# Performance work log

Hardware: AMD Instinct MI355X
Metric: run time of the kernel (lower is better)

Reference implementation:

```python
import jax, jax.numpy as jnp
import numpy as np

MAX_WORDS = 256  # = batch['labels'].shape[1]


def _align(hidden, word_ids, max_words):
    """Batched segment-mean: (B,S,D) subtoken states -> (B,max_words,D) word states.
    Equivalent to align_subtokens_to_words applied per sample (word_ids all valid)."""
    B, S, D = hidden.shape
    seg = (word_ids.astype(jnp.int32) + jnp.arange(B, dtype=jnp.int32)[:, None] * max_words).reshape(-1)
    sums = jax.ops.segment_sum(hidden.reshape(-1, D), seg, num_segments=B * max_words)
    cnts = jax.ops.segment_sum(jnp.ones((B * S,), hidden.dtype), seg, num_segments=B * max_words)
    out = jnp.where(cnts[:, None] > 0, sums / jnp.maximum(cnts, 1.0)[:, None], 0.0)
    return out.reshape(B, max_words, D)


def setup_inputs() -> dict:
    key = jax.random.key(0)
    ks = jax.random.split(key, 8)
    B, S, D, W = 64, 512, 768, MAX_WORDS
    h_hing_sub = jax.random.normal(ks[0], (B, S, D), dtype=jnp.float32)
    h_rob_sub = jax.random.normal(ks[1], (B, S, D), dtype=jnp.float32)
    hing_word_ids = jnp.sort(jax.random.randint(ks[2], (B, S), 0, W), axis=-1).astype(jnp.int32)
    rob_word_ids = jnp.sort(jax.random.randint(ks[3], (B, S), 0, W), axis=-1).astype(jnp.int32)
    num_words = jax.random.randint(ks[4], (B,), 1, W).astype(jnp.int32)
    router_w1 = jax.random.normal(ks[5], (2 * D, 256), dtype=jnp.float32) * (1.0 / np.sqrt(2 * D))
    router_b1 = jnp.zeros((256,), jnp.float32)
    router_w2 = jax.random.normal(ks[6], (256, 1), dtype=jnp.float32) * (1.0 / 16.0)
    router_b2 = jnp.zeros((1,), jnp.float32)
    head_w = jax.random.normal(ks[7], (D, 7), dtype=jnp.float32) * (1.0 / np.sqrt(D))
    head_b = jnp.zeros((7,), jnp.float32)
    return {
        'h_hing_sub': h_hing_sub, 'h_rob_sub': h_rob_sub,
        'hing_word_ids': hing_word_ids, 'rob_word_ids': rob_word_ids,
        'num_words': num_words,
        'router_w1': router_w1, 'router_b1': router_b1,
        'router_w2': router_w2, 'router_b2': router_b2,
        'head_w': head_w, 'head_b': head_b,
    }


def reference(h_hing_sub, h_rob_sub, hing_word_ids, rob_word_ids, num_words,
              router_w1, router_b1, router_w2, router_b2, head_w, head_b):
    W = MAX_WORDS
    # scatter-mean subtokens -> words (the dominant custom-kernel op)
    h_hing = _align(h_hing_sub, hing_word_ids, W)   # (B, W, 768)
    h_rob = _align(h_rob_sub, rob_word_ids, W)      # (B, W, 768)
    # token-level MLP router on concatenated word states (router_input='both')
    router_in = jnp.concatenate([h_hing, h_rob], axis=-1)             # (B, W, 1536)
    hdn = jax.nn.relu(jnp.einsum('bwd,dh->bwh', router_in, router_w1) + router_b1)
    alpha = jax.nn.sigmoid(jnp.einsum('bwh,ho->bwo', hdn, router_w2) + router_b2)  # (B, W, 1)
    blended = alpha * h_hing + (1.0 - alpha) * h_rob                  # (B, W, 768)
    logits = jnp.einsum('bwd,dl->bwl', blended, head_w) + head_b      # (B, W, num_labels)
    l2_disagreement = jnp.linalg.norm(h_hing - h_rob, axis=-1)        # (B, W)
    return logits, alpha.squeeze(-1), l2_disagreement
```

## Files before the change

kernel.cpp:

```cpp
#include <hip/hip_runtime.h>
#include <hip/hip_bf16.h>
#include <math.h>

#define BATCH 64
#define SEQ   512
#define DIM   768
#define NW    256
#define NT    (BATCH * NW)
#define KDIM  1536
#define HID   256
#define NL    7

#define BM  32
#define BK  64
#define BKP 72
#define NKT (KDIM / BK)

typedef __bf16 bf16_t;
typedef bf16_t bf16x4 __attribute__((ext_vector_type(4)));
typedef bf16_t bf16x8 __attribute__((ext_vector_type(8)));
typedef float  f32x4  __attribute__((ext_vector_type(4)));

__global__ __launch_bounds__(256) void prep_kernel(
    const float* __restrict__ w1, bf16_t* __restrict__ w1t,
    const int* __restrict__ idh, const int* __restrict__ idr,
    int* __restrict__ starts)
{
    if (blockIdx.x < 192) {
        int kc = blockIdx.x >> 3;
        int kg = blockIdx.x & 7;
        int n  = threadIdx.x;
        bf16x8 v;
        #pragma unroll
        for (int j = 0; j < 8; j++)
            v[j] = (bf16_t)w1[(size_t)(kc * 64 + kg * 8 + j) * HID + n];
        *(bf16x8*)(w1t + (size_t)kc * (HID * BK) + n * BK + kg * 8) = v;
    } else {
        int blk = blockIdx.x - 192;
        int t = blk >> 6;
        int b = blk & 63;
        const int* ids = (t ? idr : idh) + b * SEQ;
        int w = threadIdx.x;
        int lo = 0, hi = SEQ;
        while (lo < hi) {
            int m = (lo + hi) >> 1;
            if (ids[m] < w) lo = m + 1; else hi = m;
        }
        int* row = starts + blk * 257;
        row[w] = lo;
        if (w == 0) row[256] = SEQ;
    }
}

__global__ __launch_bounds__(256) void align_kernel(
    const float* __restrict__ hh, const float* __restrict__ hr,
    const int* __restrict__ starts, bf16_t* __restrict__ X)
{
    int tid  = threadIdx.x;
    int lane = tid & 63;
    int wv   = tid >> 6;
    int task = blockIdx.x * 4 + wv;
    int w    = task & 255;
    int t    = (task >> 8) & 1;
    int b    = task >> 9;

    const int* st = starts + (t * 64 + b) * 257;
    int lo = __builtin_amdgcn_readfirstlane(st[w]);
    int hi = __builtin_amdgcn_readfirstlane(st[w + 1]);
    int n  = hi - lo;

    const f32x4* src = (const f32x4*)((t ? hr : hh) + (size_t)b * SEQ * DIM) + lane;
    bf16_t*      xr  = X + (size_t)b * NW * KDIM + (size_t)w * KDIM + t * DIM;

    f32x4 a0 = {0.f,0.f,0.f,0.f}, a1 = a0, a2 = a0;
    for (int s = lo; s < hi; s++) {
        const f32x4* r = src + (size_t)s * 192;
        f32x4 v0 = r[0];
        f32x4 v1 = r[64];
        f32x4 v2 = r[128];
        a0 += v0; a1 += v1; a2 += v2;
    }
    float inv = n > 0 ? 1.0f / (float)n : 0.0f;
    bf16x4 o0, o1, o2;
    #pragma unroll
    for (int e = 0; e < 4; e++) {
        o0[e] = (bf16_t)(a0[e] * inv);
        o1[e] = (bf16_t)(a1[e] * inv);
        o2[e] = (bf16_t)(a2[e] * inv);
    }
    *(bf16x4*)(xr + lane * 4)         = o0;
    *(bf16x4*)(xr + (lane + 64) * 4)  = o1;
    *(bf16x4*)(xr + (lane + 128) * 4) = o2;
}

__global__ __launch_bounds__(256) void gemm_blend_kernel(
    const bf16_t* __restrict__ X, const bf16_t* __restrict__ w1t,
    const float* __restrict__ b1, const float* __restrict__ w2,
    const float* __restrict__ b2, const float* __restrict__ hw,
    const float* __restrict__ hb, float* __restrict__ out)
{
    __shared__ __align__(16) unsigned char smem[4608 + 36864];
    bf16_t (*Xs)[BKP] = (bf16_t (*)[BKP])smem;
    bf16_t (*Ws)[BKP] = (bf16_t (*)[BKP])(smem + 4608);
    float*  hws       = (float*)(smem + 4608);
    __shared__ float alpha_acc[BM];
    __shared__ float alpha_s[BM];

    int tid   = threadIdx.x;
    int lane  = tid & 63;
    int wv    = tid >> 6;
    int row16 = lane & 15;
    int quad  = lane >> 4;
    int tok0  = blockIdx.x * BM;

    f32x4 acc[2][4];
    #pragma unroll
    for (int mi = 0; mi < 2; mi++)
        #pragma unroll
        for (int ni = 0; ni < 4; ni++)
            acc[mi][ni] = (f32x4){0.f, 0.f, 0.f, 0.f};

    int xr = tid >> 3;
    int xc = tid & 7;

    for (int kc = 0; kc < NKT; kc++) {
        {
            const uint4* src = (const uint4*)(X + (size_t)(tok0 + xr) * KDIM + kc * BK + xc * 8);
            *(uint4*)(&Xs[xr][xc * 8]) = *src;
        }
        {
            const uint4* srcb = (const uint4*)(w1t + (size_t)kc * (HID * BK));
            #pragma unroll
            for (int i = 0; i < 8; i++) {
                int cidx = tid + i * 256;
                *(uint4*)(&Ws[cidx >> 3][(cidx & 7) * 8]) = srcb[cidx];
            }
        }
        __syncthreads();
        #pragma unroll
        for (int kk2 = 0; kk2 < 2; kk2++) {
            bf16x8 af[2], bfg[4];
            #pragma unroll
            for (int mi = 0; mi < 2; mi++)
                af[mi] = *(const bf16x8*)(&Xs[mi * 16 + row16][kk2 * 32 + quad * 8]);
            #pragma unroll
            for (int ni = 0; ni < 4; ni++)
                bfg[ni] = *(const bf16x8*)(&Ws[wv * 64 + ni * 16 + row16][kk2 * 32 + quad * 8]);
            #pragma unroll
            for (int mi = 0; mi < 2; mi++)
                #pragma unroll
                for (int ni = 0; ni < 4; ni++)
                    acc[mi][ni] = __builtin_amdgcn_mfma_f32_16x16x32_bf16(
                        af[mi], bfg[ni], acc[mi][ni], 0, 0, 0);
        }
        __syncthreads();
    }

    float w2v[4], b1v[4];
    #pragma unroll
    for (int ni = 0; ni < 4; ni++) {
        int col = wv * 64 + ni * 16 + row16;
        w2v[ni] = w2[col];
        b1v[ni] = b1[col];
    }
    if (tid < BM) alpha_acc[tid] = 0.f;
    __syncthreads();

    #pragma unroll
    for (int mi = 0; mi < 2; mi++) {
        #pragma unroll
        for (int r = 0; r < 4; r++) {
            float p = 0.f;
            #pragma unroll
            for (int ni = 0; ni < 4; ni++) {
                float v = acc[mi][ni][r] + b1v[ni];
                v = v > 0.f ? v : 0.f;
                p += v * w2v[ni];
            }
            p += __shfl_xor(p, 1);
            p += __shfl_xor(p, 2);
            p += __shfl_xor(p, 4);
            p += __shfl_xor(p, 8);
            if (row16 == 0)
                atomicAdd(&alpha_acc[mi * 16 + quad * 4 + r], p);
        }
    }

    for (int i = tid; i < DIM * NL; i += 256) {
        int d = i / NL, l = i - d * NL;
        hws[l * DIM + d] = hw[i];
    }
    __syncthreads();

    if (tid < BM) {
        float a = 1.f / (1.f + expf(-(alpha_acc[tid] + b2[0])));
        alpha_s[tid] = a;
        out[(size_t)NT * NL + tok0 + tid] = a;
    }
    __syncthreads();

    {
        int g   = lane >> 3;
        int u   = lane & 7;
        int tl  = wv * 8 + g;
        int tok = tok0 + tl;
        float a = alpha_s[tl];
        const bf16_t* xrow = X + (size_t)tok * KDIM;

        float lg[NL] = {0.f, 0.f, 0.f, 0.f, 0.f, 0.f, 0.f};
        float l2 = 0.f;

        #pragma unroll
        for (int k = 0; k < 12; k++) {
            int d0 = (k * 8 + u) * 8;
            bf16x8 hp = *(const bf16x8*)(xrow + d0);
            bf16x8 rp = *(const bf16x8*)(xrow + DIM + d0);
            float bl[8];
            #pragma unroll
            for (int e = 0; e < 8; e++) {
                float hhv = (float)hp[e];
                float hrv = (float)rp[e];
                float df  = hhv - hrv;
                bl[e] = fmaf(a, df, hrv);
                l2 = fmaf(df, df, l2);
            }
            #pragma unroll
            for (int l = 0; l < NL; l++) {
                f32x4 wA = *(const f32x4*)(&hws[l * DIM + d0]);
                f32x4 wB = *(const f32x4*)(&hws[l * DIM + d0 + 4]);
                lg[l] += bl[0]*wA[0] + bl[1]*wA[1] + bl[2]*wA[2] + bl[3]*wA[3]
                       + bl[4]*wB[0] + bl[5]*wB[1] + bl[6]*wB[2] + bl[7]*wB[3];
            }
        }

        #pragma unroll
        for (int off = 1; off < 8; off <<= 1) {
            #pragma unroll
            for (int l = 0; l < NL; l++) lg[l] += __shfl_xor(lg[l], off);
            l2 += __shfl_xor(l2, off);
        }

        if (u < NL) {
            float v = (u == 0) ? lg[0] : (u == 1) ? lg[1] : (u == 2) ? lg[2]
                    : (u == 3) ? lg[3] : (u == 4) ? lg[4] : (u == 5) ? lg[5] : lg[6];
            out[(size_t)tok * NL + u] = v + hb[u];
        } else {
            out[(size_t)NT * NL + NT + tok] = sqrtf(l2);
        }
    }
}

extern "C" void kernel_launch(void* const* d_in, const int* in_sizes, int n_in,
                              void* d_out, int out_size, void* d_ws, size_t ws_size,
                              hipStream_t stream)
{
    const float* hh  = (const float*)d_in[0];
    const float* hr  = (const float*)d_in[1];
    const int*   idh = (const int*)d_in[2];
    const int*   idr = (const int*)d_in[3];
    const float* w1  = (const float*)d_in[5];
    const float* b1  = (const float*)d_in[6];
    const float* w2  = (const float*)d_in[7];
    const float* b2  = (const float*)d_in[8];
    const float* hw  = (const float*)d_in[9];
    const float* hb  = (const float*)d_in[10];
    float* out = (float*)d_out;

    bf16_t* X      = (bf16_t*)d_ws;
    bf16_t* w1t    = X + (size_t)NT * KDIM;
    int*    starts = (int*)(w1t + (size_t)NKT * HID * BK);

    prep_kernel<<<320, 256, 0, stream>>>(w1, w1t, idh, idr, starts);
    align_kernel<<<8192, 256, 0, stream>>>(hh, hr, starts, X);
    gemm_blend_kernel<<<NT / BM, 256, 0, stream>>>(X, w1t, b1, w2, b2,
                                                   hw, hb, out);
}
```

Baseline: 283.6 us.

## Double GEMM token tile to 64 with 512-thread blocks and 4x2 wave layout

Raises the GEMM block tile from 32 to 64 tokens and doubles the block to 512 threads. Waves are rearranged into a 4x2 grid, so each wave computes one 16-row slice against 128 hidden columns. Each staged W1 tile is now reused across twice as many tokens, which halves the number of blocks and the total W1 traffic from L2. In exchange there are fewer blocks to spread across the GPU, each wave holds more accumulator registers, and blocks need more shared memory.

```diff
diff --git a/kernel.cpp b/kernel.cpp
--- a/kernel.cpp
+++ b/kernel.cpp
@@ -11,7 +11,7 @@
 #define HID   256
 #define NL    7
 
-#define BM  32
+#define BM  64
 #define BK  64
 #define BKP 72
 #define NKT (KDIM / BK)
@@ -93,32 +93,34 @@
     *(bf16x4*)(xr + (lane + 128) * 4) = o2;
 }
 
-__global__ __launch_bounds__(256) void gemm_blend_kernel(
+__global__ __launch_bounds__(512, 2) void gemm_blend_kernel(
     const bf16_t* __restrict__ X, const bf16_t* __restrict__ w1t,
     const float* __restrict__ b1, const float* __restrict__ w2,
     const float* __restrict__ b2, const float* __restrict__ hw,
     const float* __restrict__ hb, float* __restrict__ out)
 {
-    __shared__ __align__(16) unsigned char smem[4608 + 36864];
+    __shared__ __align__(16) unsigned char smem[BM * BKP * 2 + HID * BKP * 2];
     bf16_t (*Xs)[BKP] = (bf16_t (*)[BKP])smem;
-    bf16_t (*Ws)[BKP] = (bf16_t (*)[BKP])(smem + 4608);
-    float*  hws       = (float*)(smem + 4608);
+    bf16_t (*Ws)[BKP] = (bf16_t (*)[BKP])(smem + BM * BKP * 2);
+    float*  hws       = (float*)(smem + BM * BKP * 2);
     __shared__ float alpha_acc[BM];
     __shared__ float alpha_s[BM];
 
     int tid   = threadIdx.x;
     int lane  = tid & 63;
     int wv    = tid >> 6;
+    int mw    = wv >> 1;
+    int nw    = wv & 1;
     int row16 = lane & 15;
     int quad  = lane >> 4;
     int tok0  = blockIdx.x * BM;
 
-    f32x4 acc[2][4];
+    f32x4 acc[8];
     #pragma unroll
-    for (int mi = 0; mi < 2; mi++)
-        #pragma unroll
-        for (int ni = 0; ni < 4; ni++)
-            acc[mi][ni] = (f32x4){0.f, 0.f, 0.f, 0.f};
+    for (int ni = 0; ni < 8; ni++)
+        acc[ni] = (f32x4){0.f, 0.f, 0.f, 0.f};
+
+    if (tid < BM) alpha_acc[tid] = 0.f;
 
     int xr = tid >> 3;
     int xc = tid & 7;
@@ -131,49 +133,41 @@
         {
             const uint4* srcb = (const uint4*)(w1t + (size_t)kc * (HID * BK));
             #pragma unroll
-            for (int i = 0; i < 8; i++) {
-                int cidx = tid + i * 256;
+            for (int i = 0; i < 4; i++) {
+                int cidx = tid + i * 512;
                 *(uint4*)(&Ws[cidx >> 3][(cidx & 7) * 8]) = srcb[cidx];
             }
         }
         __syncthreads();
         #pragma unroll
         for (int kk2 = 0; kk2 < 2; kk2++) {
-            bf16x8 af[2], bfg[4];
-            #pragma unroll
-            for (int mi = 0; mi < 2; mi++)
-                af[mi] = *(const bf16x8*)(&Xs[mi * 16 + row16][kk2 * 32 + quad * 8]);
-            #pragma unroll
-            for (int ni = 0; ni < 4; ni++)
-                bfg[ni] = *(const bf16x8*)(&Ws[wv * 64 + ni * 16 + row16][kk2 * 32 + quad * 8]);
-            #pragma unroll
-            for (int mi = 0; mi < 2; mi++)
-                #pragma unroll
-                for (int ni = 0; ni < 4; ni++)
-                    acc[mi][ni] = __builtin_amdgcn_mfma_f32_16x16x32_bf16(
-                        af[mi], bfg[ni], acc[mi][ni], 0, 0, 0);
+            bf16x8 af, bfg[8];
+            af = *(const bf16x8*)(&Xs[mw * 16 + row16][kk2 * 32 + quad * 8]);
+            #pragma unroll
+            for (int ni = 0; ni < 8; ni++)
+                bfg[ni] = *(const bf16x8*)(&Ws[nw * 128 + ni * 16 + row16][kk2 * 32 + quad * 8]);
+            #pragma unroll
+            for (int ni = 0; ni < 8; ni++)
+                acc[ni] = __builtin_amdgcn_mfma_f32_16x16x32_bf16(
+                    af, bfg[ni], acc[ni], 0, 0, 0);
         }
         __syncthreads();
     }
 
-    float w2v[4], b1v[4];
-    #pragma unroll
-    for (int ni = 0; ni < 4; ni++) {
-        int col = wv * 64 + ni * 16 + row16;
-        w2v[ni] = w2[col];
-        b1v[ni] = b1[col];
-    }
-    if (tid < BM) alpha_acc[tid] = 0.f;
-    __syncthreads();
-
-    #pragma unroll
-    for (int mi = 0; mi < 2; mi++) {
+    {
+        float w2v[8], b1v[8];
+        #pragma unroll
+        for (int ni = 0; ni < 8; ni++) {
+            int col = nw * 128 + ni * 16 + row16;
+            w2v[ni] = w2[col];
+            b1v[ni] = b1[col];
+        }
         #pragma unroll
         for (int r = 0; r < 4; r++) {
             float p = 0.f;
             #pragma unroll
-            for (int ni = 0; ni < 4; ni++) {
-                float v = acc[mi][ni][r] + b1v[ni];
+            for (int ni = 0; ni < 8; ni++) {
+                float v = acc[ni][r] + b1v[ni];
                 v = v > 0.f ? v : 0.f;
                 p += v * w2v[ni];
             }
@@ -182,11 +176,11 @@
             p += __shfl_xor(p, 4);
             p += __shfl_xor(p, 8);
             if (row16 == 0)
-                atomicAdd(&alpha_acc[mi * 16 + quad * 4 + r], p);
-        }
-    }
-
-    for (int i = tid; i < DIM * NL; i += 256) {
+                atomicAdd(&alpha_acc[mw * 16 + quad * 4 + r], p);
+        }
+    }
+
+    for (int i = tid; i < DIM * NL; i += 512) {
         int d = i / NL, l = i - d * NL;
         hws[l * DIM + d] = hw[i];
     }
@@ -272,6 +266,6 @@
 
     prep_kernel<<<320, 256, 0, stream>>>(w1, w1t, idh, idr, starts);
     align_kernel<<<8192, 256, 0, stream>>>(hh, hr, starts, X);
-    gemm_blend_kernel<<<NT / BM, 256, 0, stream>>>(X, w1t, b1, w2, b2,
+    gemm_blend_kernel<<<NT / BM, 512, 0, stream>>>(X, w1t, b1, w2, b2,
                                                    hw, hb, out);
 }
```

Result: no change. 286.8 us (+1.1%).
